# Optimization experiments

Measured on AMD Instinct MI355X. Metric: run time of the kernel, lower is better.

Reference implementation:

```python
import jax, jax.numpy as jnp
import numpy as np

N_ATOMS = 512
N_MOL = 16
HIDDEN = 128
FILTERS = 128
NUM_RBF = 50
CUTOFF = 10.0
N_LAYERS = 3


def setup_inputs() -> dict:
    key = jax.random.key(0)
    ks = jax.random.split(key, 20)
    s = 0.05
    inp = {
        "atomic_numbers": jax.random.randint(ks[0], (N_ATOMS,), 0, 100),
        "positions": jax.random.uniform(ks[1], (N_ATOMS, 3), jnp.float32) * CUTOFF,
        "batch": jnp.sort(jax.random.randint(ks[2], (N_ATOMS,), 0, N_MOL)),
        # parameters (linear weights stored as [in, out])
        "emb": jax.random.normal(ks[3], (100, HIDDEN), jnp.float32) * s,
        "fw1": jax.random.normal(ks[4], (N_LAYERS, NUM_RBF, FILTERS), jnp.float32) * s,
        "fb1": jnp.zeros((N_LAYERS, FILTERS), jnp.float32),
        "fw2": jax.random.normal(ks[5], (N_LAYERS, FILTERS, FILTERS), jnp.float32) * s,
        "fb2": jnp.zeros((N_LAYERS, FILTERS), jnp.float32),
        "d1w": jax.random.normal(ks[6], (N_LAYERS, HIDDEN, FILTERS), jnp.float32) * s,
        "d1b": jnp.zeros((N_LAYERS, FILTERS), jnp.float32),
        "d2w": jax.random.normal(ks[7], (N_LAYERS, FILTERS, HIDDEN), jnp.float32) * s,
        "d2b": jnp.zeros((N_LAYERS, HIDDEN), jnp.float32),
        "ow1": jax.random.normal(ks[8], (HIDDEN, HIDDEN // 2), jnp.float32) * s,
        "ob1": jnp.zeros((HIDDEN // 2,), jnp.float32),
        "ow2": jax.random.normal(ks[9], (HIDDEN // 2, 1), jnp.float32) * s,
        "ob2": jnp.zeros((1,), jnp.float32),
    }
    return inp


def _schnet_fwd(atomic_numbers, positions, batch, emb, fw1, fb1, fw2, fb2,
                d1w, d1b, d2w, d2b, ow1, ob1, ow2, ob2):
    N = positions.shape[0]
    x = emb[atomic_numbers]                                  # [N, H]

    # all-pairs distances (safe sqrt for the zero diagonal)
    diff = positions[:, None, :] - positions[None, :, :]     # [N, N, 3]
    d2 = jnp.sum(diff * diff, axis=-1)                       # [N, N]
    d = jnp.sqrt(jnp.where(d2 > 0, d2, 1.0))
    d = jnp.where(d2 > 0, d, 0.0)

    eye = jnp.eye(N, dtype=bool)
    valid = (~eye) & (d < CUTOFF)                            # no self-edges, within cutoff

    # gaussian RBF embedding of distances
    centers = jnp.linspace(0.0, CUTOFF, NUM_RBF)             # [R]
    width = CUTOFF / NUM_RBF
    rbf = jnp.exp(-((d[..., None] - centers) ** 2) / (2.0 * width * width))  # [N, N, R]

    # cosine cutoff envelope; zero on invalid edges -> messages identical to edge-list version
    env = 0.5 * (jnp.cos(d * jnp.pi / CUTOFF) + 1.0) * valid.astype(d.dtype)  # [N, N]

    for l in range(N_LAYERS):
        filt = jax.nn.silu(rbf @ fw1[l] + fb1[l]) @ fw2[l] + fb2[l]   # [N, N, F]
        filt = filt * env[..., None]
        xj = x @ d1w[l] + d1b[l]                                      # [N, F] source features
        # message[i,j] = xj[i] * filt[i,j]; scatter-add to destination j
        agg = jnp.einsum('if,ijf->jf', xj, filt)                      # [N, F]
        x = x + agg @ d2w[l] + d2b[l]

    # mean-pool atoms per molecule
    mol_sum = jax.ops.segment_sum(x, batch, num_segments=N_MOL)       # [M, H]
    counts = jax.ops.segment_sum(jnp.ones((N,), x.dtype), batch, num_segments=N_MOL)
    mol = mol_sum / jnp.clip(counts, 1.0)[:, None]

    h = jax.nn.silu(mol @ ow1 + ob1)
    return h @ ow2 + ob2                                              # [M, 1]


def reference(atomic_numbers, positions, batch, emb, fw1, fb1, fw2, fb2,
              d1w, d1b, d2w, d2b, ow1, ob1, ow2, ob2):
    return _schnet_fwd(atomic_numbers, positions, batch, emb, fw1, fb1, fw2, fb2,
                       d1w, d1b, d2w, d2b, ow1, ob1, ow2, ob2)
```

## Files before the change

kernel.cpp:

```cpp
#include <hip/hip_runtime.h>
#include <math.h>

#define N_ATOMS 512
#define N_MOL   16
#define HIDDEN  128
#define FILTERS 128
#define NUM_RBF 50
#define CUTOFF  10.0f
#define N_LAYERS 3

#define KB4    4096
#define NB4    (KB4 + 1)
#define TBPL   129
#define TBLK   (N_LAYERS * TBPL)
#define EMBB   16
#define PI_F   3.14159265358979f
#define DINV   409.6f
#define DSTEP  (CUTOFF / (float)KB4)

__device__ __forceinline__ unsigned short f2bf(float v) {
    unsigned u = __float_as_uint(v);
    u += 0x7fffu + ((u >> 16) & 1u);
    return (unsigned short)(u >> 16);
}

__global__ void __launch_bounds__(256) k_front(
        const int* __restrict__ an, const float* __restrict__ emb,
        const float* __restrict__ d1w, const float* __restrict__ d1b,
        const float* __restrict__ fw1, const float* __restrict__ fb1,
        const float* __restrict__ fw2, const float* __restrict__ fb2,
        float* __restrict__ x, unsigned short* __restrict__ xj,
        unsigned short* __restrict__ tab, float* __restrict__ molsum,
        int* __restrict__ done) {
    __shared__ float s_rbf[32][NUM_RBF];
    __shared__ __align__(16) float s_H[32][132];
    __shared__ __align__(16) float s_row[32][HIDDEN];
    __shared__ int   s_an[32];
    int bid = blockIdx.x, t = threadIdx.x;

    if (bid == 0) {
        for (int idx = t; idx < N_MOL * HIDDEN; idx += 256) molsum[idx] = 0.f;
        if (t == 0) *done = 0;
    }

    int cq = t & 31, ag = t >> 5;

    if (bid < TBLK) {
        int l = bid / TBPL, bx = bid - l * TBPL;
        int bin0 = bx * 32;
        const float* w1g = fw1 + (size_t)l * NUM_RBF * FILTERS;
        const float* w2g = fw2 + (size_t)l * FILTERS * FILTERS;
        for (int idx = t; idx < 32 * NUM_RBF; idx += 256) {
            int lb = idx / NUM_RBF, r = idx - lb * NUM_RBF;
            float dd = (bin0 + lb) * DSTEP;
            float cr = r * (CUTOFF / (float)(NUM_RBF - 1));
            float xx = dd - cr;
            s_rbf[lb][r] = __expf(-xx * xx * 12.5f);
        }
        __syncthreads();
        {
            float h[4][4];
            float4 bv = *(const float4*)(fb1 + (size_t)l * FILTERS + 4 * cq);
            float bva[4] = { bv.x, bv.y, bv.z, bv.w };
            #pragma unroll
            for (int aa = 0; aa < 4; aa++)
                #pragma unroll
                for (int cc = 0; cc < 4; cc++) h[aa][cc] = bva[cc];
            #pragma unroll 2
            for (int r = 0; r < NUM_RBF; r++) {
                float4 w = *(const float4*)(w1g + (size_t)r * FILTERS + 4 * cq);
                float wa[4] = { w.x, w.y, w.z, w.w };
                #pragma unroll
                for (int aa = 0; aa < 4; aa++) {
                    float rb = s_rbf[ag * 4 + aa][r];
                    #pragma unroll
                    for (int cc = 0; cc < 4; cc++) h[aa][cc] = fmaf(rb, wa[cc], h[aa][cc]);
                }
            }
            __syncthreads();
            #pragma unroll
            for (int aa = 0; aa < 4; aa++) {
                float4 sv;
                sv.x = h[aa][0] / (1.f + __expf(-h[aa][0]));
                sv.y = h[aa][1] / (1.f + __expf(-h[aa][1]));
                sv.z = h[aa][2] / (1.f + __expf(-h[aa][2]));
                sv.w = h[aa][3] / (1.f + __expf(-h[aa][3]));
                *(float4*)(&s_H[ag * 4 + aa][4 * cq]) = sv;
            }
        }
        __syncthreads();
        float o[4][4];
        float4 b2v = *(const float4*)(fb2 + (size_t)l * FILTERS + 4 * cq);
        float b2a[4] = { b2v.x, b2v.y, b2v.z, b2v.w };
        #pragma unroll
        for (int aa = 0; aa < 4; aa++)
            #pragma unroll
            for (int cc = 0; cc < 4; cc++) o[aa][cc] = b2a[cc];
        #pragma unroll 4
        for (int hh = 0; hh < FILTERS; hh += 2) {
            float4 wA = *(const float4*)(w2g + (size_t)hh * FILTERS + 4 * cq);
            float4 wB = *(const float4*)(w2g + (size_t)(hh + 1) * FILTERS + 4 * cq);
            float wa[4] = { wA.x, wA.y, wA.z, wA.w };
            float wb[4] = { wB.x, wB.y, wB.z, wB.w };
            #pragma unroll
            for (int aa = 0; aa < 4; aa++) {
                float2 hp = *(const float2*)(&s_H[ag * 4 + aa][hh]);
                #pragma unroll
                for (int cc = 0; cc < 4; cc++) {
                    o[aa][cc] = fmaf(hp.x, wa[cc], o[aa][cc]);
                    o[aa][cc] = fmaf(hp.y, wb[cc], o[aa][cc]);
                }
            }
        }
        size_t base = (size_t)l * NB4 * FILTERS;
        #pragma unroll
        for (int aa = 0; aa < 4; aa++) {
            int bin = bin0 + ag * 4 + aa;
            if (bin <= KB4) {
                float dd = bin * DSTEP;
                float env = (bin >= KB4) ? 0.f : 0.5f * (__cosf(dd * (PI_F / CUTOFF)) + 1.f);
                #pragma unroll
                for (int cp = 0; cp < 2; cp++) {
                    unsigned int pk = (unsigned)f2bf(o[aa][2 * cp] * env) |
                                      ((unsigned)f2bf(o[aa][2 * cp + 1] * env) << 16);
                    *(unsigned int*)(tab + base + (size_t)bin * FILTERS + 4 * cq + 2 * cp) = pk;
                }
            }
        }
    } else {
        int eb = bid - TBLK;
        int i0 = eb * 32;
        if (t < 32) s_an[t] = an[i0 + t];
        __syncthreads();
        for (int idx = t; idx < 32 * HIDDEN; idx += 256) {
            int a = idx >> 7, c = idx & 127;
            float v = emb[(size_t)s_an[a] * HIDDEN + c];
            s_row[a][c] = v;
            x[(size_t)(i0 + a) * HIDDEN + c] = v;
        }
        __syncthreads();
        float o[4][4];
        float4 bv = *(const float4*)(d1b + 4 * cq);
        float bva[4] = { bv.x, bv.y, bv.z, bv.w };
        #pragma unroll
        for (int aa = 0; aa < 4; aa++)
            #pragma unroll
            for (int cc = 0; cc < 4; cc++) o[aa][cc] = bva[cc];
        #pragma unroll 4
        for (int h = 0; h < HIDDEN; h += 2) {
            float4 wA = *(const float4*)(d1w + (size_t)h * FILTERS + 4 * cq);
            float4 wB = *(const float4*)(d1w + (size_t)(h + 1) * FILTERS + 4 * cq);
            float wa[4] = { wA.x, wA.y, wA.z, wA.w };
            float wb[4] = { wB.x, wB.y, wB.z, wB.w };
            #pragma unroll
            for (int aa = 0; aa < 4; aa++) {
                float2 hp = *(const float2*)(&s_row[ag * 4 + aa][h]);
                #pragma unroll
                for (int cc = 0; cc < 4; cc++) {
                    o[aa][cc] = fmaf(hp.x, wa[cc], o[aa][cc]);
                    o[aa][cc] = fmaf(hp.y, wb[cc], o[aa][cc]);
                }
            }
        }
        #pragma unroll
        for (int aa = 0; aa < 4; aa++) {
            int i = i0 + ag * 4 + aa;
            #pragma unroll
            for (int cp = 0; cp < 2; cp++) {
                unsigned int pk = (unsigned)f2bf(o[aa][2 * cp]) |
                                  ((unsigned)f2bf(o[aa][2 * cp + 1]) << 16);
                *(unsigned int*)(xj + (size_t)i * FILTERS + 4 * cq + 2 * cp) = pk;
            }
        }
    }
}

template<int LAST>
__global__ void __launch_bounds__(512) k_layer(const float* __restrict__ pos,
        const unsigned int* __restrict__ tabl, const unsigned int* __restrict__ xj_in,
        float* __restrict__ x, const float* __restrict__ w2, const float* __restrict__ b2,
        const float* __restrict__ w1n, const float* __restrict__ b1n,
        unsigned short* __restrict__ xj_out,
        const int* __restrict__ batch, float* __restrict__ molsum, int* __restrict__ done,
        const float* __restrict__ ow1, const float* __restrict__ ob1,
        const float* __restrict__ ow2, const float* __restrict__ ob2,
        float* __restrict__ out) {
    int bid = blockIdx.x, t = threadIdx.x;
    int j0 = 2 * bid, j1 = j0 + 1;
    int wv = t >> 6, e = t & 63;
    __shared__ unsigned int s_bin[N_ATOMS];
    __shared__ float s_part[2][8][FILTERS];
    __shared__ float s_red[4][FILTERS];
    __shared__ float s_agg[2][FILTERS];
    __shared__ float s_xn[2][HIDDEN];
    __shared__ int   s_cnt;
    {
        float px = pos[3*t], py = pos[3*t+1], pz = pos[3*t+2];
        float ax = pos[3*j0], ay = pos[3*j0+1], az = pos[3*j0+2];
        float bx = pos[3*j1], by = pos[3*j1+1], bz = pos[3*j1+2];
        float d0 = sqrtf((px-ax)*(px-ax) + (py-ay)*(py-ay) + (pz-az)*(pz-az));
        float d1 = sqrtf((px-bx)*(px-bx) + (py-by)*(py-by) + (pz-bz)*(pz-bz));
        unsigned int b0 = (t == j0 || d0 >= CUTOFF) ? KB4 : (unsigned)(int)fmaf(d0, DINV, 0.5f);
        unsigned int b1 = (t == j1 || d1 >= CUTOFF) ? KB4 : (unsigned)(int)fmaf(d1, DINV, 0.5f);
        if (b0 > KB4) b0 = KB4;
        if (b1 > KB4) b1 = KB4;
        s_bin[t] = b0 | (b1 << 16);
    }
    int c = t & 127, seg = t >> 7, jj = seg >> 1, sub = seg & 1;
    float xold = (sub == 0) ? x[(size_t)(jj ? j1 : j0) * HIDDEN + c] : 0.f;
    __syncthreads();
    float a0e = 0.f, a0o = 0.f, a1e = 0.f, a1o = 0.f;
    int i0 = wv * 64;
    for (int ii = 0; ii < 64; ii += 4) {
        #pragma unroll
        for (int r = 0; r < 4; r++) {
            unsigned int pk = s_bin[i0 + ii + r];
            unsigned int bb0 = pk & 0xffffu, bb1 = pk >> 16;
            unsigned int xu = xj_in[(size_t)(i0 + ii + r) * 64 + e];
            unsigned int f0 = tabl[(size_t)bb0 * 64 + e];
            unsigned int f1 = tabl[(size_t)bb1 * 64 + e];
            float xe = __uint_as_float(xu << 16), xo = __uint_as_float(xu & 0xffff0000u);
            float p0e = __uint_as_float(f0 << 16), p0o = __uint_as_float(f0 & 0xffff0000u);
            float p1e = __uint_as_float(f1 << 16), p1o = __uint_as_float(f1 & 0xffff0000u);
            a0e = fmaf(xe, p0e, a0e);  a0o = fmaf(xo, p0o, a0o);
            a1e = fmaf(xe, p1e, a1e);  a1o = fmaf(xo, p1o, a1o);
        }
    }
    s_part[0][wv][2*e] = a0e;  s_part[0][wv][2*e+1] = a0o;
    s_part[1][wv][2*e] = a1e;  s_part[1][wv][2*e+1] = a1o;
    __syncthreads();
    if (t < 256) {
        int pj = t >> 7, cc = t & 127;
        float s = 0.f;
        #pragma unroll
        for (int w8 = 0; w8 < 8; w8++) s += s_part[pj][w8][cc];
        s_agg[pj][cc] = s;
    }
    __syncthreads();
    float v = 0.f;
    #pragma unroll 8
    for (int ff = sub * 64; ff < sub * 64 + 64; ff++)
        v = fmaf(s_agg[jj][ff], w2[(size_t)ff * HIDDEN + c], v);
    s_red[seg][c] = v;
    __syncthreads();
    float xnew = 0.f;
    if (sub == 0) {
        xnew = xold + b2[c] + s_red[jj*2][c] + s_red[jj*2+1][c];
        x[(size_t)(jj ? j1 : j0) * HIDDEN + c] = xnew;
        s_xn[jj][c] = xnew;
    }
    __syncthreads();
    if (!LAST) {
        float a2 = 0.f;
        #pragma unroll 8
        for (int hh = sub * 64; hh < sub * 64 + 64; hh++)
            a2 = fmaf(s_xn[jj][hh], w1n[(size_t)hh * FILTERS + c], a2);
        s_red[seg][c] = a2;
        __syncthreads();
        if (sub == 0)
            xj_out[(size_t)(jj ? j1 : j0) * FILTERS + c] =
                f2bf(b1n[c] + s_red[jj*2][c] + s_red[jj*2+1][c]);
    } else {
        if (sub == 0) atomicAdd(&molsum[(size_t)batch[jj ? j1 : j0] * HIDDEN + c], xnew);
        __syncthreads();
        if (t == 0) atomicAdd(done, 1);
        if (bid < N_MOL) {
            int m = bid;
            if (t == 0) {
                while (atomicAdd(done, 0) < N_ATOMS / 2) __builtin_amdgcn_s_sleep(16);
                s_cnt = 0;
            }
            __syncthreads();
            atomicAdd(&s_cnt, (batch[t] == m) ? 1 : 0);
            __syncthreads();
            int cnt = s_cnt;
            if (t < HIDDEN)
                s_xn[0][t] = atomicAdd(&molsum[(size_t)m * HIDDEN + t], 0.f)
                           / (float)(cnt > 0 ? cnt : 1);
            __syncthreads();
            int o = t & 63, sl = t >> 6;
            float a = 0.f;
            #pragma unroll 8
            for (int h = sl * 16; h < sl * 16 + 16; h++)
                a = fmaf(s_xn[0][h], ow1[h * 64 + o], a);
            float* sr = (float*)s_part;
            sr[sl * 64 + o] = a;
            __syncthreads();
            if (t < 64) {
                float vv = ob1[t];
                #pragma unroll
                for (int s8 = 0; s8 < 8; s8++) vv += sr[s8 * 64 + t];
                float hh = vv / (1.f + __expf(-vv));
                float d2 = hh * ow2[t];
                for (int off = 32; off > 0; off >>= 1) d2 += __shfl_down(d2, off, 64);
                if (t == 0) out[m] = d2 + ob2[0];
            }
        }
    }
}

extern "C" void kernel_launch(void* const* d_in, const int* in_sizes, int n_in,
                              void* d_out, int out_size, void* d_ws, size_t ws_size,
                              hipStream_t stream) {
    const int*   an    = (const int*)  d_in[0];
    const float* pos   = (const float*)d_in[1];
    const int*   batch = (const int*)  d_in[2];
    const float* emb   = (const float*)d_in[3];
    const float* fw1   = (const float*)d_in[4];
    const float* fb1   = (const float*)d_in[5];
    const float* fw2   = (const float*)d_in[6];
    const float* fb2   = (const float*)d_in[7];
    const float* d1w   = (const float*)d_in[8];
    const float* d1b   = (const float*)d_in[9];
    const float* d2w   = (const float*)d_in[10];
    const float* d2b   = (const float*)d_in[11];
    const float* ow1   = (const float*)d_in[12];
    const float* ob1   = (const float*)d_in[13];
    const float* ow2   = (const float*)d_in[14];
    const float* ob2   = (const float*)d_in[15];
    float* out = (float*)d_out;

    float*          x    = (float*)d_ws;
    unsigned short* xjA  = (unsigned short*)(x + N_ATOMS * HIDDEN);
    unsigned short* xjB  = xjA + (size_t)N_ATOMS * FILTERS;
    unsigned short* tab  = xjB + (size_t)N_ATOMS * FILTERS;
    float*          mols = (float*)(tab + (size_t)N_LAYERS * NB4 * FILTERS);
    int*            done = (int*)(mols + N_MOL * HIDDEN);

    k_front<<<TBLK + EMBB, 256, 0, stream>>>(
        an, emb, d1w, d1b, fw1, fb1, fw2, fb2, x, xjA, tab, mols, done);

    const unsigned int* t0 = (const unsigned int*)(tab + (size_t)0 * NB4 * FILTERS);
    const unsigned int* t1 = (const unsigned int*)(tab + (size_t)1 * NB4 * FILTERS);
    const unsigned int* t2 = (const unsigned int*)(tab + (size_t)2 * NB4 * FILTERS);

    k_layer<0><<<N_ATOMS/2, 512, 0, stream>>>(pos, t0, (const unsigned int*)xjA, x,
        d2w + (size_t)0*FILTERS*HIDDEN, d2b + (size_t)0*HIDDEN,
        d1w + (size_t)1*HIDDEN*FILTERS, d1b + (size_t)1*FILTERS, xjB,
        batch, mols, done, ow1, ob1, ow2, ob2, out);
    k_layer<0><<<N_ATOMS/2, 512, 0, stream>>>(pos, t1, (const unsigned int*)xjB, x,
        d2w + (size_t)1*FILTERS*HIDDEN, d2b + (size_t)1*HIDDEN,
        d1w + (size_t)2*HIDDEN*FILTERS, d1b + (size_t)2*FILTERS, xjA,
        batch, mols, done, ow1, ob1, ow2, ob2, out);
    k_layer<1><<<N_ATOMS/2, 512, 0, stream>>>(pos, t2, (const unsigned int*)xjA, x,
        d2w + (size_t)2*FILTERS*HIDDEN, d2b + (size_t)2*HIDDEN,
        d1w, d1b, xjB,
        batch, mols, done, ow1, ob1, ow2, ob2, out);
}
```

Measured before the change: 63.93 us.

## Fuse three layer kernels into one persistent kernel with grid barriers

Replaces three per-layer kernel launches with a single kernel that loops over the layers and synchronises all 256 blocks through per-layer atomic counters. Node features stay in registers across layers, and the next-layer source features are exchanged through agent-scope atomic stores and loads. This removes two launch gaps and the global write/read of x between layers. In exchange it relies on all 256 blocks being co-resident for the spin barrier, and it adds spin-wait latency at each layer.

```diff
diff --git a/kernel.cpp b/kernel.cpp
--- a/kernel.cpp
+++ b/kernel.cpp
@@ -14,6 +14,7 @@
 #define TBPL   129
 #define TBLK   (N_LAYERS * TBPL)
 #define EMBB   16
+#define NBLK   (N_ATOMS / 2)
 #define PI_F   3.14159265358979f
 #define DINV   409.6f
 #define DSTEP  (CUTOFF / (float)KB4)
@@ -40,7 +41,7 @@
 
     if (bid == 0) {
         for (int idx = t; idx < N_MOL * HIDDEN; idx += 256) molsum[idx] = 0.f;
-        if (t == 0) *done = 0;
+        if (t < 4) done[t] = 0;
     }
 
     int cq = t & 31, ag = t >> 5;
@@ -175,18 +176,18 @@
     }
 }
 
-template<int LAST>
-__global__ void __launch_bounds__(512) k_layer(const float* __restrict__ pos,
-        const unsigned int* __restrict__ tabl, const unsigned int* __restrict__ xj_in,
-        float* __restrict__ x, const float* __restrict__ w2, const float* __restrict__ b2,
-        const float* __restrict__ w1n, const float* __restrict__ b1n,
-        unsigned short* __restrict__ xj_out,
+__global__ void __launch_bounds__(512) k_layers(const float* __restrict__ pos,
+        const unsigned int* __restrict__ tabu, const unsigned int* __restrict__ xj0,
+        unsigned int* __restrict__ xj1, unsigned int* __restrict__ xj2,
+        const float* __restrict__ x,
+        const float* __restrict__ d2w, const float* __restrict__ d2b,
+        const float* __restrict__ d1w, const float* __restrict__ d1b,
         const int* __restrict__ batch, float* __restrict__ molsum, int* __restrict__ done,
         const float* __restrict__ ow1, const float* __restrict__ ob1,
         const float* __restrict__ ow2, const float* __restrict__ ob2,
         float* __restrict__ out) {
     int bid = blockIdx.x, t = threadIdx.x;
-    int j0 = 2 * bid, j1 = j0 + 1;
+    int j0a = 2 * bid, j1a = j0a + 1;
     int wv = t >> 6, e = t & 63;
     __shared__ unsigned int s_bin[N_ATOMS];
     __shared__ float s_part[2][8][FILTERS];
@@ -196,105 +197,148 @@
     __shared__ int   s_cnt;
     {
         float px = pos[3*t], py = pos[3*t+1], pz = pos[3*t+2];
-        float ax = pos[3*j0], ay = pos[3*j0+1], az = pos[3*j0+2];
-        float bx = pos[3*j1], by = pos[3*j1+1], bz = pos[3*j1+2];
+        float ax = pos[3*j0a], ay = pos[3*j0a+1], az = pos[3*j0a+2];
+        float bx = pos[3*j1a], by = pos[3*j1a+1], bz = pos[3*j1a+2];
         float d0 = sqrtf((px-ax)*(px-ax) + (py-ay)*(py-ay) + (pz-az)*(pz-az));
         float d1 = sqrtf((px-bx)*(px-bx) + (py-by)*(py-by) + (pz-bz)*(pz-bz));
-        unsigned int b0 = (t == j0 || d0 >= CUTOFF) ? KB4 : (unsigned)(int)fmaf(d0, DINV, 0.5f);
-        unsigned int b1 = (t == j1 || d1 >= CUTOFF) ? KB4 : (unsigned)(int)fmaf(d1, DINV, 0.5f);
+        unsigned int b0 = (t == j0a || d0 >= CUTOFF) ? KB4 : (unsigned)(int)fmaf(d0, DINV, 0.5f);
+        unsigned int b1 = (t == j1a || d1 >= CUTOFF) ? KB4 : (unsigned)(int)fmaf(d1, DINV, 0.5f);
         if (b0 > KB4) b0 = KB4;
         if (b1 > KB4) b1 = KB4;
         s_bin[t] = b0 | (b1 << 16);
     }
     int c = t & 127, seg = t >> 7, jj = seg >> 1, sub = seg & 1;
-    float xold = (sub == 0) ? x[(size_t)(jj ? j1 : j0) * HIDDEN + c] : 0.f;
+    int jmy = jj ? j1a : j0a;
+    float xcur = (sub == 0) ? x[(size_t)jmy * HIDDEN + c] : 0.f;
     __syncthreads();
-    float a0e = 0.f, a0o = 0.f, a1e = 0.f, a1o = 0.f;
-    int i0 = wv * 64;
-    for (int ii = 0; ii < 64; ii += 4) {
-        #pragma unroll
-        for (int r = 0; r < 4; r++) {
-            unsigned int pk = s_bin[i0 + ii + r];
-            unsigned int bb0 = pk & 0xffffu, bb1 = pk >> 16;
-            unsigned int xu = xj_in[(size_t)(i0 + ii + r) * 64 + e];
-            unsigned int f0 = tabl[(size_t)bb0 * 64 + e];
-            unsigned int f1 = tabl[(size_t)bb1 * 64 + e];
-            float xe = __uint_as_float(xu << 16), xo = __uint_as_float(xu & 0xffff0000u);
-            float p0e = __uint_as_float(f0 << 16), p0o = __uint_as_float(f0 & 0xffff0000u);
-            float p1e = __uint_as_float(f1 << 16), p1o = __uint_as_float(f1 & 0xffff0000u);
-            a0e = fmaf(xe, p0e, a0e);  a0o = fmaf(xo, p0o, a0o);
-            a1e = fmaf(xe, p1e, a1e);  a1o = fmaf(xo, p1o, a1o);
-        }
-    }
-    s_part[0][wv][2*e] = a0e;  s_part[0][wv][2*e+1] = a0o;
-    s_part[1][wv][2*e] = a1e;  s_part[1][wv][2*e+1] = a1o;
+
+    for (int l = 0; l < N_LAYERS; l++) {
+        const unsigned int* tabl = tabu + (size_t)l * NB4 * 64;
+        const unsigned int* xin  = (l == 0) ? xj0 : (l == 1) ? xj1 : xj2;
+        float a0e = 0.f, a0o = 0.f, a1e = 0.f, a1o = 0.f;
+        int i0 = wv * 64;
+        if (l == 0) {
+            for (int ii = 0; ii < 64; ii += 4) {
+                #pragma unroll
+                for (int r = 0; r < 4; r++) {
+                    unsigned int pk = s_bin[i0 + ii + r];
+                    unsigned int bb0 = pk & 0xffffu, bb1 = pk >> 16;
+                    unsigned int xu = xin[(size_t)(i0 + ii + r) * 64 + e];
+                    unsigned int f0 = tabl[(size_t)bb0 * 64 + e];
+                    unsigned int f1 = tabl[(size_t)bb1 * 64 + e];
+                    float xe = __uint_as_float(xu << 16), xo = __uint_as_float(xu & 0xffff0000u);
+                    float p0e = __uint_as_float(f0 << 16), p0o = __uint_as_float(f0 & 0xffff0000u);
+                    float p1e = __uint_as_float(f1 << 16), p1o = __uint_as_float(f1 & 0xffff0000u);
+                    a0e = fmaf(xe, p0e, a0e);  a0o = fmaf(xo, p0o, a0o);
+                    a1e = fmaf(xe, p1e, a1e);  a1o = fmaf(xo, p1o, a1o);
+                }
+            }
+        } else {
+            for (int ii = 0; ii < 64; ii += 4) {
+                #pragma unroll
+                for (int r = 0; r < 4; r++) {
+                    unsigned int pk = s_bin[i0 + ii + r];
+                    unsigned int bb0 = pk & 0xffffu, bb1 = pk >> 16;
+                    unsigned int xu = __hip_atomic_load(&xin[(size_t)(i0 + ii + r) * 64 + e],
+                                        __ATOMIC_RELAXED, __HIP_MEMORY_SCOPE_AGENT);
+                    unsigned int f0 = tabl[(size_t)bb0 * 64 + e];
+                    unsigned int f1 = tabl[(size_t)bb1 * 64 + e];
+                    float xe = __uint_as_float(xu << 16), xo = __uint_as_float(xu & 0xffff0000u);
+                    float p0e = __uint_as_float(f0 << 16), p0o = __uint_as_float(f0 & 0xffff0000u);
+                    float p1e = __uint_as_float(f1 << 16), p1o = __uint_as_float(f1 & 0xffff0000u);
+                    a0e = fmaf(xe, p0e, a0e);  a0o = fmaf(xo, p0o, a0o);
+                    a1e = fmaf(xe, p1e, a1e);  a1o = fmaf(xo, p1o, a1o);
+                }
+            }
+        }
+        s_part[0][wv][2*e] = a0e;  s_part[0][wv][2*e+1] = a0o;
+        s_part[1][wv][2*e] = a1e;  s_part[1][wv][2*e+1] = a1o;
+        __syncthreads();
+        if (t < 256) {
+            int pj = t >> 7, cc = t & 127;
+            float s = 0.f;
+            #pragma unroll
+            for (int w8 = 0; w8 < 8; w8++) s += s_part[pj][w8][cc];
+            s_agg[pj][cc] = s;
+        }
+        __syncthreads();
+        const float* w2 = d2w + (size_t)l * FILTERS * HIDDEN;
+        const float* b2 = d2b + (size_t)l * HIDDEN;
+        float v = 0.f;
+        #pragma unroll 8
+        for (int ff = sub * 64; ff < sub * 64 + 64; ff++)
+            v = fmaf(s_agg[jj][ff], w2[(size_t)ff * HIDDEN + c], v);
+        s_red[seg][c] = v;
+        __syncthreads();
+        if (sub == 0) {
+            xcur = xcur + b2[c] + s_red[jj*2][c] + s_red[jj*2+1][c];
+            s_xn[jj][c] = xcur;
+        }
+        __syncthreads();
+        if (l < N_LAYERS - 1) {
+            const float* w1n = d1w + (size_t)(l + 1) * HIDDEN * FILTERS;
+            const float* b1n = d1b + (size_t)(l + 1) * FILTERS;
+            float a2 = 0.f;
+            #pragma unroll 8
+            for (int hh = sub * 64; hh < sub * 64 + 64; hh++)
+                a2 = fmaf(s_xn[jj][hh], w1n[(size_t)hh * FILTERS + c], a2);
+            s_red[seg][c] = a2;
+            __syncthreads();
+            if (sub == 0) s_agg[jj][c] = b1n[c] + s_red[jj*2][c] + s_red[jj*2+1][c];
+            __syncthreads();
+            unsigned int* xout = (l == 0) ? xj1 : xj2;
+            if (t < 128) {
+                int row = t >> 6, ee = t & 63;
+                unsigned int pk = (unsigned)f2bf(s_agg[row][2*ee]) |
+                                  ((unsigned)f2bf(s_agg[row][2*ee+1]) << 16);
+                __hip_atomic_store(&xout[(size_t)(j0a + row) * 64 + ee], pk,
+                                   __ATOMIC_RELAXED, __HIP_MEMORY_SCOPE_AGENT);
+            }
+            __syncthreads();
+            if (t == 0) {
+                atomicAdd(&done[l], 1);
+                while (__hip_atomic_load(&done[l], __ATOMIC_RELAXED,
+                                         __HIP_MEMORY_SCOPE_AGENT) < NBLK)
+                    __builtin_amdgcn_s_sleep(16);
+            }
+            __syncthreads();
+        }
+    }
+    if (sub == 0) atomicAdd(&molsum[(size_t)batch[jmy] * HIDDEN + c], xcur);
     __syncthreads();
-    if (t < 256) {
-        int pj = t >> 7, cc = t & 127;
-        float s = 0.f;
-        #pragma unroll
-        for (int w8 = 0; w8 < 8; w8++) s += s_part[pj][w8][cc];
-        s_agg[pj][cc] = s;
-    }
-    __syncthreads();
-    float v = 0.f;
-    #pragma unroll 8
-    for (int ff = sub * 64; ff < sub * 64 + 64; ff++)
-        v = fmaf(s_agg[jj][ff], w2[(size_t)ff * HIDDEN + c], v);
-    s_red[seg][c] = v;
-    __syncthreads();
-    float xnew = 0.f;
-    if (sub == 0) {
-        xnew = xold + b2[c] + s_red[jj*2][c] + s_red[jj*2+1][c];
-        x[(size_t)(jj ? j1 : j0) * HIDDEN + c] = xnew;
-        s_xn[jj][c] = xnew;
-    }
-    __syncthreads();
-    if (!LAST) {
-        float a2 = 0.f;
+    if (t == 0) atomicAdd(&done[2], 1);
+    if (bid < N_MOL) {
+        int m = bid;
+        if (t == 0) {
+            while (__hip_atomic_load(&done[2], __ATOMIC_RELAXED,
+                                     __HIP_MEMORY_SCOPE_AGENT) < NBLK)
+                __builtin_amdgcn_s_sleep(16);
+            s_cnt = 0;
+        }
+        __syncthreads();
+        atomicAdd(&s_cnt, (batch[t] == m) ? 1 : 0);
+        __syncthreads();
+        int cnt = s_cnt;
+        if (t < HIDDEN)
+            s_xn[0][t] = atomicAdd(&molsum[(size_t)m * HIDDEN + t], 0.f)
+                       / (float)(cnt > 0 ? cnt : 1);
+        __syncthreads();
+        int o = t & 63, sl = t >> 6;
+        float a = 0.f;
         #pragma unroll 8
-        for (int hh = sub * 64; hh < sub * 64 + 64; hh++)
-            a2 = fmaf(s_xn[jj][hh], w1n[(size_t)hh * FILTERS + c], a2);
-        s_red[seg][c] = a2;
-        __syncthreads();
-        if (sub == 0)
-            xj_out[(size_t)(jj ? j1 : j0) * FILTERS + c] =
-                f2bf(b1n[c] + s_red[jj*2][c] + s_red[jj*2+1][c]);
-    } else {
-        if (sub == 0) atomicAdd(&molsum[(size_t)batch[jj ? j1 : j0] * HIDDEN + c], xnew);
-        __syncthreads();
-        if (t == 0) atomicAdd(done, 1);
-        if (bid < N_MOL) {
-            int m = bid;
-            if (t == 0) {
-                while (atomicAdd(done, 0) < N_ATOMS / 2) __builtin_amdgcn_s_sleep(16);
-                s_cnt = 0;
-            }
-            __syncthreads();
-            atomicAdd(&s_cnt, (batch[t] == m) ? 1 : 0);
-            __syncthreads();
-            int cnt = s_cnt;
-            if (t < HIDDEN)
-                s_xn[0][t] = atomicAdd(&molsum[(size_t)m * HIDDEN + t], 0.f)
-                           / (float)(cnt > 0 ? cnt : 1);
-            __syncthreads();
-            int o = t & 63, sl = t >> 6;
-            float a = 0.f;
-            #pragma unroll 8
-            for (int h = sl * 16; h < sl * 16 + 16; h++)
-                a = fmaf(s_xn[0][h], ow1[h * 64 + o], a);
-            float* sr = (float*)s_part;
-            sr[sl * 64 + o] = a;
-            __syncthreads();
-            if (t < 64) {
-                float vv = ob1[t];
-                #pragma unroll
-                for (int s8 = 0; s8 < 8; s8++) vv += sr[s8 * 64 + t];
-                float hh = vv / (1.f + __expf(-vv));
-                float d2 = hh * ow2[t];
-                for (int off = 32; off > 0; off >>= 1) d2 += __shfl_down(d2, off, 64);
-                if (t == 0) out[m] = d2 + ob2[0];
-            }
+        for (int h = sl * 16; h < sl * 16 + 16; h++)
+            a = fmaf(s_xn[0][h], ow1[h * 64 + o], a);
+        float* sr = (float*)s_part;
+        sr[sl * 64 + o] = a;
+        __syncthreads();
+        if (t < 64) {
+            float vv = ob1[t];
+            #pragma unroll
+            for (int s8 = 0; s8 < 8; s8++) vv += sr[s8 * 64 + t];
+            float hh = vv / (1.f + __expf(-vv));
+            float d2 = hh * ow2[t];
+            for (int off = 32; off > 0; off >>= 1) d2 += __shfl_down(d2, off, 64);
+            if (t == 0) out[m] = d2 + ob2[0];
         }
     }
 }
@@ -321,29 +365,17 @@
     float* out = (float*)d_out;
 
     float*          x    = (float*)d_ws;
-    unsigned short* xjA  = (unsigned short*)(x + N_ATOMS * HIDDEN);
-    unsigned short* xjB  = xjA + (size_t)N_ATOMS * FILTERS;
-    unsigned short* tab  = xjB + (size_t)N_ATOMS * FILTERS;
+    unsigned short* xj0  = (unsigned short*)(x + N_ATOMS * HIDDEN);
+    unsigned int*   xj1  = (unsigned int*)(xj0 + (size_t)N_ATOMS * FILTERS);
+    unsigned int*   xj2  = xj1 + (size_t)N_ATOMS * 64;
+    unsigned short* tab  = (unsigned short*)(xj2 + (size_t)N_ATOMS * 64);
     float*          mols = (float*)(tab + (size_t)N_LAYERS * NB4 * FILTERS);
     int*            done = (int*)(mols + N_MOL * HIDDEN);
 
     k_front<<<TBLK + EMBB, 256, 0, stream>>>(
-        an, emb, d1w, d1b, fw1, fb1, fw2, fb2, x, xjA, tab, mols, done);
-
-    const unsigned int* t0 = (const unsigned int*)(tab + (size_t)0 * NB4 * FILTERS);
-    const unsigned int* t1 = (const unsigned int*)(tab + (size_t)1 * NB4 * FILTERS);
-    const unsigned int* t2 = (const unsigned int*)(tab + (size_t)2 * NB4 * FILTERS);
-
-    k_layer<0><<<N_ATOMS/2, 512, 0, stream>>>(pos, t0, (const unsigned int*)xjA, x,
-        d2w + (size_t)0*FILTERS*HIDDEN, d2b + (size_t)0*HIDDEN,
-        d1w + (size_t)1*HIDDEN*FILTERS, d1b + (size_t)1*FILTERS, xjB,
-        batch, mols, done, ow1, ob1, ow2, ob2, out);
-    k_layer<0><<<N_ATOMS/2, 512, 0, stream>>>(pos, t1, (const unsigned int*)xjB, x,
-        d2w + (size_t)1*FILTERS*HIDDEN, d2b + (size_t)1*HIDDEN,
-        d1w + (size_t)2*HIDDEN*FILTERS, d1b + (size_t)2*FILTERS, xjA,
-        batch, mols, done, ow1, ob1, ow2, ob2, out);
-    k_layer<1><<<N_ATOMS/2, 512, 0, stream>>>(pos, t2, (const unsigned int*)xjA, x,
-        d2w + (size_t)2*FILTERS*HIDDEN, d2b + (size_t)2*HIDDEN,
-        d1w, d1b, xjB,
-        batch, mols, done, ow1, ob1, ow2, ob2, out);
+        an, emb, d1w, d1b, fw1, fb1, fw2, fb2, x, xj0, tab, mols, done);
+
+    k_layers<<<NBLK, 512, 0, stream>>>(pos, (const unsigned int*)tab,
+        (const unsigned int*)xj0, xj1, xj2, x,
+        d2w, d2b, d1w, d1b, batch, mols, done, ow1, ob1, ow2, ob2, out);
 }
```

After: 74.80 us. +17.0%, slower.

## Halve filter table, one atom per block, last-block-done readout, L2 table prefetch

Applied to the files above, without the earlier changes.

The filter lookup table is halved to 2048 distance bins, so the precompute kernel launches fewer blocks and the table is smaller to cache. Each layer kernel now handles one destination atom per block instead of two, doubling the grid to 512 blocks. Each block also XOR-reads a slice of the table to warm L2 before the gather loop. The final readout drops the spin-wait by the first 16 blocks: the last block to arrive, found with an atomic ticket, computes all 16 molecule outputs. Coarser bins add interpolation error to the filters, and the prefetch adds extra global reads per block.

```diff
diff --git a/kernel.cpp b/kernel.cpp
--- a/kernel.cpp
+++ b/kernel.cpp
@@ -9,14 +9,15 @@
 #define CUTOFF  10.0f
 #define N_LAYERS 3
 
-#define KB4    4096
-#define NB4    (KB4 + 1)
-#define TBPL   129
+#define KB2    2048
+#define NB2    (KB2 + 1)
+#define TBPL   65
 #define TBLK   (N_LAYERS * TBPL)
 #define EMBB   16
 #define PI_F   3.14159265358979f
-#define DINV   409.6f
-#define DSTEP  (CUTOFF / (float)KB4)
+#define DINV   204.8f
+#define DSTEP  (CUTOFF / (float)KB2)
+#define TAB_U4 ((NB2 * 64) / 4)
 
 __device__ __forceinline__ unsigned short f2bf(float v) {
     unsigned u = __float_as_uint(v);
@@ -40,7 +41,7 @@
 
     if (bid == 0) {
         for (int idx = t; idx < N_MOL * HIDDEN; idx += 256) molsum[idx] = 0.f;
-        if (t == 0) *done = 0;
+        if (t < 4) done[t] = 0;
     }
 
     int cq = t & 31, ag = t >> 5;
@@ -112,13 +113,13 @@
                 }
             }
         }
-        size_t base = (size_t)l * NB4 * FILTERS;
+        size_t base = (size_t)l * NB2 * FILTERS;
         #pragma unroll
         for (int aa = 0; aa < 4; aa++) {
             int bin = bin0 + ag * 4 + aa;
-            if (bin <= KB4) {
+            if (bin <= KB2) {
                 float dd = bin * DSTEP;
-                float env = (bin >= KB4) ? 0.f : 0.5f * (__cosf(dd * (PI_F / CUTOFF)) + 1.f);
+                float env = (bin >= KB2) ? 0.f : 0.5f * (__cosf(dd * (PI_F / CUTOFF)) + 1.f);
                 #pragma unroll
                 for (int cp = 0; cp < 2; cp++) {
                     unsigned int pk = (unsigned)f2bf(o[aa][2 * cp] * env) |
@@ -180,120 +181,126 @@
         const unsigned int* __restrict__ tabl, const unsigned int* __restrict__ xj_in,
         float* __restrict__ x, const float* __restrict__ w2, const float* __restrict__ b2,
         const float* __restrict__ w1n, const float* __restrict__ b1n,
-        unsigned short* __restrict__ xj_out,
+        unsigned int* __restrict__ xj_out,
         const int* __restrict__ batch, float* __restrict__ molsum, int* __restrict__ done,
         const float* __restrict__ ow1, const float* __restrict__ ob1,
         const float* __restrict__ ow2, const float* __restrict__ ob2,
         float* __restrict__ out) {
-    int bid = blockIdx.x, t = threadIdx.x;
-    int j0 = 2 * bid, j1 = j0 + 1;
+    int j = blockIdx.x, t = threadIdx.x;
     int wv = t >> 6, e = t & 63;
-    __shared__ unsigned int s_bin[N_ATOMS];
-    __shared__ float s_part[2][8][FILTERS];
+    __shared__ unsigned short s_bin[N_ATOMS];
+    __shared__ float s_part[8][FILTERS];
     __shared__ float s_red[4][FILTERS];
-    __shared__ float s_agg[2][FILTERS];
-    __shared__ float s_xn[2][HIDDEN];
-    __shared__ int   s_cnt;
+    __shared__ float s_agg[FILTERS];
+    __shared__ float s_xn[HIDDEN];
+    __shared__ int   s_tick;
+    __shared__ float s_mol[16][HIDDEN];
+    __shared__ float s_h[16][64];
+    __shared__ int   s_c16[16];
     {
         float px = pos[3*t], py = pos[3*t+1], pz = pos[3*t+2];
-        float ax = pos[3*j0], ay = pos[3*j0+1], az = pos[3*j0+2];
-        float bx = pos[3*j1], by = pos[3*j1+1], bz = pos[3*j1+2];
-        float d0 = sqrtf((px-ax)*(px-ax) + (py-ay)*(py-ay) + (pz-az)*(pz-az));
-        float d1 = sqrtf((px-bx)*(px-bx) + (py-by)*(py-by) + (pz-bz)*(pz-bz));
-        unsigned int b0 = (t == j0 || d0 >= CUTOFF) ? KB4 : (unsigned)(int)fmaf(d0, DINV, 0.5f);
-        unsigned int b1 = (t == j1 || d1 >= CUTOFF) ? KB4 : (unsigned)(int)fmaf(d1, DINV, 0.5f);
-        if (b0 > KB4) b0 = KB4;
-        if (b1 > KB4) b1 = KB4;
-        s_bin[t] = b0 | (b1 << 16);
-    }
-    int c = t & 127, seg = t >> 7, jj = seg >> 1, sub = seg & 1;
-    float xold = (sub == 0) ? x[(size_t)(jj ? j1 : j0) * HIDDEN + c] : 0.f;
-    __syncthreads();
-    float a0e = 0.f, a0o = 0.f, a1e = 0.f, a1o = 0.f;
+        float ax = pos[3*j], ay = pos[3*j+1], az = pos[3*j+2];
+        float d = sqrtf((px-ax)*(px-ax) + (py-ay)*(py-ay) + (pz-az)*(pz-az));
+        unsigned int b = (t == j || d >= CUTOFF) ? KB2 : (unsigned)(int)fmaf(d, DINV, 0.5f);
+        if (b > KB2) b = KB2;
+        s_bin[t] = (unsigned short)b;
+    }
+    int c = t & 127, seg = t >> 7;
+    float xold = (seg == 0) ? x[(size_t)j * HIDDEN + c] : 0.f;
+    {
+        const uint4* t4 = (const uint4*)tabl;
+        int slice = (j >> 3) & 31;
+        int q0 = slice * 1025;
+        int qe = q0 + 1025; if (qe > TAB_U4) qe = TAB_U4;
+        unsigned int acc = 0;
+        for (int q = q0 + t; q < qe; q += 512) {
+            uint4 w = t4[q];
+            acc ^= w.x ^ w.y ^ w.z ^ w.w;
+        }
+        asm volatile("" :: "v"(acc));
+    }
+    __syncthreads();
+    float ae = 0.f, ao = 0.f;
     int i0 = wv * 64;
-    for (int ii = 0; ii < 64; ii += 4) {
-        #pragma unroll
-        for (int r = 0; r < 4; r++) {
-            unsigned int pk = s_bin[i0 + ii + r];
-            unsigned int bb0 = pk & 0xffffu, bb1 = pk >> 16;
+    for (int ii = 0; ii < 64; ii += 8) {
+        #pragma unroll
+        for (int r = 0; r < 8; r++) {
+            int bb = s_bin[i0 + ii + r];
             unsigned int xu = xj_in[(size_t)(i0 + ii + r) * 64 + e];
-            unsigned int f0 = tabl[(size_t)bb0 * 64 + e];
-            unsigned int f1 = tabl[(size_t)bb1 * 64 + e];
+            unsigned int f  = tabl[(size_t)bb * 64 + e];
             float xe = __uint_as_float(xu << 16), xo = __uint_as_float(xu & 0xffff0000u);
-            float p0e = __uint_as_float(f0 << 16), p0o = __uint_as_float(f0 & 0xffff0000u);
-            float p1e = __uint_as_float(f1 << 16), p1o = __uint_as_float(f1 & 0xffff0000u);
-            a0e = fmaf(xe, p0e, a0e);  a0o = fmaf(xo, p0o, a0o);
-            a1e = fmaf(xe, p1e, a1e);  a1o = fmaf(xo, p1o, a1o);
-        }
-    }
-    s_part[0][wv][2*e] = a0e;  s_part[0][wv][2*e+1] = a0o;
-    s_part[1][wv][2*e] = a1e;  s_part[1][wv][2*e+1] = a1o;
-    __syncthreads();
-    if (t < 256) {
-        int pj = t >> 7, cc = t & 127;
+            float pe = __uint_as_float(f << 16),  po = __uint_as_float(f & 0xffff0000u);
+            ae = fmaf(xe, pe, ae);
+            ao = fmaf(xo, po, ao);
+        }
+    }
+    s_part[wv][2*e] = ae;  s_part[wv][2*e+1] = ao;
+    __syncthreads();
+    if (t < FILTERS) {
         float s = 0.f;
         #pragma unroll
-        for (int w8 = 0; w8 < 8; w8++) s += s_part[pj][w8][cc];
-        s_agg[pj][cc] = s;
+        for (int w8 = 0; w8 < 8; w8++) s += s_part[w8][t];
+        s_agg[t] = s;
     }
     __syncthreads();
     float v = 0.f;
     #pragma unroll 8
-    for (int ff = sub * 64; ff < sub * 64 + 64; ff++)
-        v = fmaf(s_agg[jj][ff], w2[(size_t)ff * HIDDEN + c], v);
+    for (int ff = seg * 32; ff < seg * 32 + 32; ff++)
+        v = fmaf(s_agg[ff], w2[(size_t)ff * HIDDEN + c], v);
     s_red[seg][c] = v;
     __syncthreads();
     float xnew = 0.f;
-    if (sub == 0) {
-        xnew = xold + b2[c] + s_red[jj*2][c] + s_red[jj*2+1][c];
-        x[(size_t)(jj ? j1 : j0) * HIDDEN + c] = xnew;
-        s_xn[jj][c] = xnew;
+    if (seg == 0) {
+        xnew = xold + b2[c] + s_red[0][c] + s_red[1][c] + s_red[2][c] + s_red[3][c];
+        x[(size_t)j * HIDDEN + c] = xnew;
+        s_xn[c] = xnew;
     }
     __syncthreads();
     if (!LAST) {
         float a2 = 0.f;
         #pragma unroll 8
-        for (int hh = sub * 64; hh < sub * 64 + 64; hh++)
-            a2 = fmaf(s_xn[jj][hh], w1n[(size_t)hh * FILTERS + c], a2);
+        for (int hh = seg * 32; hh < seg * 32 + 32; hh++)
+            a2 = fmaf(s_xn[hh], w1n[(size_t)hh * FILTERS + c], a2);
         s_red[seg][c] = a2;
         __syncthreads();
-        if (sub == 0)
-            xj_out[(size_t)(jj ? j1 : j0) * FILTERS + c] =
-                f2bf(b1n[c] + s_red[jj*2][c] + s_red[jj*2+1][c]);
+        if (t < 64) {
+            float v0 = b1n[2*t]   + s_red[0][2*t]   + s_red[1][2*t]   + s_red[2][2*t]   + s_red[3][2*t];
+            float v1 = b1n[2*t+1] + s_red[0][2*t+1] + s_red[1][2*t+1] + s_red[2][2*t+1] + s_red[3][2*t+1];
+            xj_out[(size_t)j * 64 + t] = (unsigned)f2bf(v0) | ((unsigned)f2bf(v1) << 16);
+        }
     } else {
-        if (sub == 0) atomicAdd(&molsum[(size_t)batch[jj ? j1 : j0] * HIDDEN + c], xnew);
-        __syncthreads();
-        if (t == 0) atomicAdd(done, 1);
-        if (bid < N_MOL) {
-            int m = bid;
-            if (t == 0) {
-                while (atomicAdd(done, 0) < N_ATOMS / 2) __builtin_amdgcn_s_sleep(16);
-                s_cnt = 0;
-            }
-            __syncthreads();
-            atomicAdd(&s_cnt, (batch[t] == m) ? 1 : 0);
-            __syncthreads();
-            int cnt = s_cnt;
-            if (t < HIDDEN)
-                s_xn[0][t] = atomicAdd(&molsum[(size_t)m * HIDDEN + t], 0.f)
-                           / (float)(cnt > 0 ? cnt : 1);
-            __syncthreads();
-            int o = t & 63, sl = t >> 6;
-            float a = 0.f;
-            #pragma unroll 8
-            for (int h = sl * 16; h < sl * 16 + 16; h++)
-                a = fmaf(s_xn[0][h], ow1[h * 64 + o], a);
-            float* sr = (float*)s_part;
-            sr[sl * 64 + o] = a;
-            __syncthreads();
-            if (t < 64) {
-                float vv = ob1[t];
-                #pragma unroll
-                for (int s8 = 0; s8 < 8; s8++) vv += sr[s8 * 64 + t];
-                float hh = vv / (1.f + __expf(-vv));
-                float d2 = hh * ow2[t];
-                for (int off = 32; off > 0; off >>= 1) d2 += __shfl_down(d2, off, 64);
-                if (t == 0) out[m] = d2 + ob2[0];
+        if (seg == 0) atomicAdd(&molsum[(size_t)batch[j] * HIDDEN + c], xnew);
+        __syncthreads();
+        if (t == 0) s_tick = atomicAdd(&done[0], 1);
+        __syncthreads();
+        if (s_tick == (int)gridDim.x - 1) {
+            if (t < 16) s_c16[t] = 0;
+            __syncthreads();
+            atomicAdd(&s_c16[batch[t]], 1);
+            __syncthreads();
+            #pragma unroll
+            for (int mo = 0; mo < 4; mo++) {
+                int m = mo * 4 + seg;
+                float sv = atomicAdd(&molsum[(size_t)m * HIDDEN + c], 0.f);
+                int cnt = s_c16[m];
+                s_mol[m][c] = sv / (float)(cnt > 0 ? cnt : 1);
+            }
+            __syncthreads();
+            #pragma unroll
+            for (int rr = 0; rr < 2; rr++) {
+                int o = t + rr * 512;
+                int m = o >> 6, k = o & 63;
+                float a = ob1[k];
+                #pragma unroll 8
+                for (int h = 0; h < HIDDEN; h++) a = fmaf(s_mol[m][h], ow1[h * 64 + k], a);
+                s_h[m][k] = a / (1.f + __expf(-a));
+            }
+            __syncthreads();
+            if (t < N_MOL) {
+                float a = ob2[0];
+                #pragma unroll 8
+                for (int h = 0; h < 64; h++) a = fmaf(s_h[t][h], ow2[h], a);
+                out[t] = a;
             }
         }
     }
@@ -321,29 +328,30 @@
     float* out = (float*)d_out;
 
     float*          x    = (float*)d_ws;
-    unsigned short* xjA  = (unsigned short*)(x + N_ATOMS * HIDDEN);
-    unsigned short* xjB  = xjA + (size_t)N_ATOMS * FILTERS;
-    unsigned short* tab  = xjB + (size_t)N_ATOMS * FILTERS;
-    float*          mols = (float*)(tab + (size_t)N_LAYERS * NB4 * FILTERS);
+    unsigned int*   xj0  = (unsigned int*)(x + N_ATOMS * HIDDEN);
+    unsigned int*   xj1  = xj0 + (size_t)N_ATOMS * 64;
+    unsigned int*   xj2  = xj1 + (size_t)N_ATOMS * 64;
+    unsigned short* tab  = (unsigned short*)(xj2 + (size_t)N_ATOMS * 64);
+    float*          mols = (float*)(tab + (size_t)N_LAYERS * NB2 * FILTERS);
     int*            done = (int*)(mols + N_MOL * HIDDEN);
 
     k_front<<<TBLK + EMBB, 256, 0, stream>>>(
-        an, emb, d1w, d1b, fw1, fb1, fw2, fb2, x, xjA, tab, mols, done);
-
-    const unsigned int* t0 = (const unsigned int*)(tab + (size_t)0 * NB4 * FILTERS);
-    const unsigned int* t1 = (const unsigned int*)(tab + (size_t)1 * NB4 * FILTERS);
-    const unsigned int* t2 = (const unsigned int*)(tab + (size_t)2 * NB4 * FILTERS);
-
-    k_layer<0><<<N_ATOMS/2, 512, 0, stream>>>(pos, t0, (const unsigned int*)xjA, x,
+        an, emb, d1w, d1b, fw1, fb1, fw2, fb2, x, (unsigned short*)xj0, tab, mols, done);
+
+    const unsigned int* t0 = (const unsigned int*)(tab + (size_t)0 * NB2 * FILTERS);
+    const unsigned int* t1 = (const unsigned int*)(tab + (size_t)1 * NB2 * FILTERS);
+    const unsigned int* t2 = (const unsigned int*)(tab + (size_t)2 * NB2 * FILTERS);
+
+    k_layer<0><<<N_ATOMS, 512, 0, stream>>>(pos, t0, xj0, x,
         d2w + (size_t)0*FILTERS*HIDDEN, d2b + (size_t)0*HIDDEN,
-        d1w + (size_t)1*HIDDEN*FILTERS, d1b + (size_t)1*FILTERS, xjB,
+        d1w + (size_t)1*HIDDEN*FILTERS, d1b + (size_t)1*FILTERS, xj1,
         batch, mols, done, ow1, ob1, ow2, ob2, out);
-    k_layer<0><<<N_ATOMS/2, 512, 0, stream>>>(pos, t1, (const unsigned int*)xjB, x,
+    k_layer<0><<<N_ATOMS, 512, 0, stream>>>(pos, t1, xj1, x,
         d2w + (size_t)1*FILTERS*HIDDEN, d2b + (size_t)1*HIDDEN,
-        d1w + (size_t)2*HIDDEN*FILTERS, d1b + (size_t)2*FILTERS, xjA,
+        d1w + (size_t)2*HIDDEN*FILTERS, d1b + (size_t)2*FILTERS, xj2,
         batch, mols, done, ow1, ob1, ow2, ob2, out);
-    k_layer<1><<<N_ATOMS/2, 512, 0, stream>>>(pos, t2, (const unsigned int*)xjA, x,
+    k_layer<1><<<N_ATOMS, 512, 0, stream>>>(pos, t2, xj2, x,
         d2w + (size_t)2*FILTERS*HIDDEN, d2b + (size_t)2*HIDDEN,
-        d1w, d1b, xjB,
+        d1w, d1b, xj0,
         batch, mols, done, ow1, ob1, ow2, ob2, out);
 }
```

After: 59.54 us, median of 2. 6.9% less time.
